# Performance work log

Hardware: AMD Instinct MI355X
Metric: run time of the kernel (lower is better)

Reference implementation:

```python
import jax, jax.numpy as jnp
import numpy as np

MARGIN = 0.3
MIN_POS_DIST = 0.1
PUSH_SCALE = 2.0
DISSIMILAR_REL = 1  # dissimilar_relation_ids == {1}


def setup_inputs() -> dict:
    key = jax.random.key(0)
    k1, k2, k3, k4, k5 = jax.random.split(key, 5)
    B, D = 16384, 1024
    h = jax.random.normal(k1, (B, D), dtype=jnp.float32)
    t = jax.random.normal(k2, (B, D), dtype=jnp.float32)
    r = jax.random.normal(k3, (B, D), dtype=jnp.float32)
    relation_ids = jax.random.randint(k4, (B,), 0, 10, dtype=jnp.int64 if jax.config.jax_enable_x64 else jnp.int32)
    neg = jax.random.randint(k5, (B,), 0, B, dtype=relation_ids.dtype)
    idx = jnp.arange(B, dtype=neg.dtype)
    neg_idx = jnp.where(neg == idx, (neg + 1) % B, neg)  # enforce neg_idx[i] != i
    return {"h": h, "t": t, "r": r, "relation_ids": relation_ids, "neg_idx": neg_idx}


def reference(h, t, r, relation_ids, neg_idx):
    # pos_dist[i] = ||h[i] + r[i] - t[i]||_2
    hr = h + r                                  # [B, D]
    pos_dist = jnp.linalg.norm(hr - t, axis=-1)  # [B]
    # neg_dist[i] = ||h[i] + r[i] - t[neg_idx[i]]||_2
    neg_dist = jnp.linalg.norm(hr - t[neg_idx], axis=-1)  # [B]

    dissim = relation_ids == DISSIMILAR_REL
    curr_margin = MARGIN * PUSH_SCALE
    loss_dissim = jax.nn.relu(curr_margin - pos_dist) + 0.5 * jnp.exp(-pos_dist)
    loss_sim = jax.nn.relu(pos_dist - neg_dist + MARGIN) + 0.3 * jax.nn.relu(MIN_POS_DIST - pos_dist)
    per_sample = jnp.where(dissim, loss_dissim, loss_sim)
    return jnp.mean(per_sample)
```

## Files before the change

### kernel.cpp

```cpp
#include <hip/hip_runtime.h>
#include <math.h>


#define BDIM 16384
#define DDIM 1024

__global__ __launch_bounds__(256) void triplet_rows_kernel(
    const float* __restrict__ h, const float* __restrict__ t,
    const float* __restrict__ r, const int* __restrict__ rel,
    const int* __restrict__ neg, float* __restrict__ per_row)
{
    const int wave = threadIdx.x >> 6;
    const int lane = threadIdx.x & 63;
    const int row  = (blockIdx.x << 2) + wave;

    const float4* h4 = (const float4*)(h + (size_t)row * DDIM);
    const float4* t4 = (const float4*)(t + (size_t)row * DDIM);
    const float4* r4 = (const float4*)(r + (size_t)row * DDIM);
    const int nidx   = neg[row];
    const float4* n4 = (const float4*)(t + (size_t)nidx * DDIM);

    float psum = 0.0f, nsum = 0.0f;
#pragma unroll
    for (int j = 0; j < 4; ++j) {
        const int k = lane + (j << 6);
        float4 hv = h4[k];
        float4 rv = r4[k];
        float4 tv = t4[k];
        float4 nv = n4[k];
        float hrx = hv.x + rv.x, hry = hv.y + rv.y,
              hrz = hv.z + rv.z, hrw = hv.w + rv.w;
        float dx = hrx - tv.x, dy = hry - tv.y,
              dz = hrz - tv.z, dw = hrw - tv.w;
        psum += dx * dx + dy * dy + dz * dz + dw * dw;
        float ex = hrx - nv.x, ey = hry - nv.y,
              ez = hrz - nv.z, ew = hrw - nv.w;
        nsum += ex * ex + ey * ey + ez * ez + ew * ew;
    }

#pragma unroll
    for (int off = 32; off > 0; off >>= 1) {
        psum += __shfl_down(psum, off, 64);
        nsum += __shfl_down(nsum, off, 64);
    }

    if (lane == 0) {
        float pos = sqrtf(psum);
        float negd = sqrtf(nsum);
        float loss;
        if (rel[row] == 1) {
            loss = fmaxf(0.6f - pos, 0.0f) + 0.5f * expf(-pos);
        } else {
            loss = fmaxf(pos - negd + 0.3f, 0.0f)
                 + 0.3f * fmaxf(0.1f - pos, 0.0f);
        }
        per_row[row] = loss;
    }
}

__global__ __launch_bounds__(256) void reduce_mean_kernel(
    const float* __restrict__ per_row, float* __restrict__ out)
{
    __shared__ float sm[4];
    float s = 0.0f;
    for (int i = threadIdx.x; i < BDIM; i += 256)
        s += per_row[i];
#pragma unroll
    for (int off = 32; off > 0; off >>= 1)
        s += __shfl_down(s, off, 64);
    const int lane = threadIdx.x & 63;
    const int wave = threadIdx.x >> 6;
    if (lane == 0) sm[wave] = s;
    __syncthreads();
    if (threadIdx.x == 0)
        out[0] = (sm[0] + sm[1] + sm[2] + sm[3]) * (1.0f / (float)BDIM);
}

extern "C" void kernel_launch(void* const* d_in, const int* in_sizes, int n_in,
                              void* d_out, int out_size, void* d_ws, size_t ws_size,
                              hipStream_t stream) {
    const float* h = (const float*)d_in[0];
    const float* t = (const float*)d_in[1];
    const float* r = (const float*)d_in[2];
    const int* rel = (const int*)d_in[3];
    const int* neg = (const int*)d_in[4];
    float* per_row = (float*)d_ws;
    float* out = (float*)d_out;

    triplet_rows_kernel<<<BDIM / 4, 256, 0, stream>>>(h, t, r, rel, neg, per_row);
    reduce_mean_kernel<<<1, 256, 0, stream>>>(per_row, out);
}
```

Before: 216.4 us.

## Fuse mean reduction via atomics, process two rows per wave, skip unused negative loads

Folds the separate reduce kernel into the row kernel by having each block atomically add its scaled partial sum into the output, which is zeroed by a tiny kernel first. Each wave now handles two rows for more memory-level parallelism per wave. For dissimilar-relation rows, whose loss ignores the negative distance, the negative pointer is aliased to the row's own t, so the random gather of a negative row is replaced by a re-read of data already being fetched. The atomic float accumulation makes the summation order nondeterministic.

Result: faster. 207.3 us (-4.2%).

```diff
diff --git a/kernel.cpp b/kernel.cpp
--- a/kernel.cpp
+++ b/kernel.cpp
@@ -4,76 +4,77 @@
 
 #define BDIM 16384
 #define DDIM 1024
+#define NBLOCK 2048
 
-__global__ __launch_bounds__(256) void triplet_rows_kernel(
+__global__ void zero_out_kernel(float* __restrict__ out) { out[0] = 0.0f; }
+
+__global__ __launch_bounds__(256) void triplet_fused_kernel(
     const float* __restrict__ h, const float* __restrict__ t,
     const float* __restrict__ r, const int* __restrict__ rel,
-    const int* __restrict__ neg, float* __restrict__ per_row)
+    const int* __restrict__ neg, float* __restrict__ out)
 {
     const int wave = threadIdx.x >> 6;
     const int lane = threadIdx.x & 63;
-    const int row  = (blockIdx.x << 2) + wave;
+    const int wid  = (blockIdx.x << 2) + wave;
+    const int row0 = wid << 1;
+    const int row1 = row0 + 1;
 
-    const float4* h4 = (const float4*)(h + (size_t)row * DDIM);
-    const float4* t4 = (const float4*)(t + (size_t)row * DDIM);
-    const float4* r4 = (const float4*)(r + (size_t)row * DDIM);
-    const int nidx   = neg[row];
-    const float4* n4 = (const float4*)(t + (size_t)nidx * DDIM);
+    const float4* h0 = (const float4*)(h + (size_t)row0 * DDIM);
+    const float4* r0 = (const float4*)(r + (size_t)row0 * DDIM);
+    const float4* t0 = (const float4*)(t + (size_t)row0 * DDIM);
+    const float4* h1 = (const float4*)(h + (size_t)row1 * DDIM);
+    const float4* r1 = (const float4*)(r + (size_t)row1 * DDIM);
+    const float4* t1 = (const float4*)(t + (size_t)row1 * DDIM);
 
-    float psum = 0.0f, nsum = 0.0f;
+    const int rel0 = rel[row0];
+    const int rel1 = rel[row1];
+    const float4* n0 = (rel0 == 1) ? t0 : (const float4*)(t + (size_t)neg[row0] * DDIM);
+    const float4* n1 = (rel1 == 1) ? t1 : (const float4*)(t + (size_t)neg[row1] * DDIM);
+
+    float ps0 = 0.0f, ns0 = 0.0f, ps1 = 0.0f, ns1 = 0.0f;
 #pragma unroll
     for (int j = 0; j < 4; ++j) {
         const int k = lane + (j << 6);
-        float4 hv = h4[k];
-        float4 rv = r4[k];
-        float4 tv = t4[k];
-        float4 nv = n4[k];
-        float hrx = hv.x + rv.x, hry = hv.y + rv.y,
-              hrz = hv.z + rv.z, hrw = hv.w + rv.w;
-        float dx = hrx - tv.x, dy = hry - tv.y,
-              dz = hrz - tv.z, dw = hrw - tv.w;
-        psum += dx * dx + dy * dy + dz * dz + dw * dw;
-        float ex = hrx - nv.x, ey = hry - nv.y,
-              ez = hrz - nv.z, ew = hrw - nv.w;
-        nsum += ex * ex + ey * ey + ez * ez + ew * ew;
+        float4 ha = h0[k]; float4 ra = r0[k]; float4 ta = t0[k]; float4 na = n0[k];
+        float4 hb = h1[k]; float4 rb = r1[k]; float4 tb = t1[k]; float4 nb = n1[k];
+
+        float ax = ha.x + ra.x, ay = ha.y + ra.y, az = ha.z + ra.z, aw = ha.w + ra.w;
+        float dx = ax - ta.x, dy = ay - ta.y, dz = az - ta.z, dw = aw - ta.w;
+        ps0 += dx * dx + dy * dy + dz * dz + dw * dw;
+        float ex = ax - na.x, ey = ay - na.y, ez = az - na.z, ew = aw - na.w;
+        ns0 += ex * ex + ey * ey + ez * ez + ew * ew;
+
+        float bx = hb.x + rb.x, by = hb.y + rb.y, bz = hb.z + rb.z, bw = hb.w + rb.w;
+        float fx = bx - tb.x, fy = by - tb.y, fz = bz - tb.z, fw = bw - tb.w;
+        ps1 += fx * fx + fy * fy + fz * fz + fw * fw;
+        float gx = bx - nb.x, gy = by - nb.y, gz = bz - nb.z, gw = bw - nb.w;
+        ns1 += gx * gx + gy * gy + gz * gz + gw * gw;
     }
 
 #pragma unroll
     for (int off = 32; off > 0; off >>= 1) {
-        psum += __shfl_down(psum, off, 64);
-        nsum += __shfl_down(nsum, off, 64);
+        ps0 += __shfl_down(ps0, off, 64);
+        ns0 += __shfl_down(ns0, off, 64);
+        ps1 += __shfl_down(ps1, off, 64);
+        ns1 += __shfl_down(ns1, off, 64);
     }
 
+    __shared__ float sm[4];
     if (lane == 0) {
-        float pos = sqrtf(psum);
-        float negd = sqrtf(nsum);
-        float loss;
-        if (rel[row] == 1) {
-            loss = fmaxf(0.6f - pos, 0.0f) + 0.5f * expf(-pos);
-        } else {
-            loss = fmaxf(pos - negd + 0.3f, 0.0f)
-                 + 0.3f * fmaxf(0.1f - pos, 0.0f);
-        }
-        per_row[row] = loss;
+        float pos0 = sqrtf(ps0), neg0 = sqrtf(ns0);
+        float pos1 = sqrtf(ps1), neg1 = sqrtf(ns1);
+        float l0, l1;
+        if (rel0 == 1) l0 = fmaxf(0.6f - pos0, 0.0f) + 0.5f * expf(-pos0);
+        else           l0 = fmaxf(pos0 - neg0 + 0.3f, 0.0f) + 0.3f * fmaxf(0.1f - pos0, 0.0f);
+        if (rel1 == 1) l1 = fmaxf(0.6f - pos1, 0.0f) + 0.5f * expf(-pos1);
+        else           l1 = fmaxf(pos1 - neg1 + 0.3f, 0.0f) + 0.3f * fmaxf(0.1f - pos1, 0.0f);
+        sm[wave] = l0 + l1;
     }
-}
-
-__global__ __launch_bounds__(256) void reduce_mean_kernel(
-    const float* __restrict__ per_row, float* __restrict__ out)
-{
-    __shared__ float sm[4];
-    float s = 0.0f;
-    for (int i = threadIdx.x; i < BDIM; i += 256)
-        s += per_row[i];
-#pragma unroll
-    for (int off = 32; off > 0; off >>= 1)
-        s += __shfl_down(s, off, 64);
-    const int lane = threadIdx.x & 63;
-    const int wave = threadIdx.x >> 6;
-    if (lane == 0) sm[wave] = s;
     __syncthreads();
-    if (threadIdx.x == 0)
-        out[0] = (sm[0] + sm[1] + sm[2] + sm[3]) * (1.0f / (float)BDIM);
+    if (threadIdx.x == 0) {
+        float blk = (sm[0] + sm[1] + sm[2] + sm[3]) * (1.0f / (float)BDIM);
+        atomicAdd(out, blk);
+    }
 }
 
 extern "C" void kernel_launch(void* const* d_in, const int* in_sizes, int n_in,
@@ -84,9 +85,8 @@
     const float* r = (const float*)d_in[2];
     const int* rel = (const int*)d_in[3];
     const int* neg = (const int*)d_in[4];
-    float* per_row = (float*)d_ws;
     float* out = (float*)d_out;
 
-    triplet_rows_kernel<<<BDIM / 4, 256, 0, stream>>>(h, t, r, rel, neg, per_row);
-    reduce_mean_kernel<<<1, 256, 0, stream>>>(per_row, out);
+    zero_out_kernel<<<1, 1, 0, stream>>>(out);
+    triplet_fused_kernel<<<NBLOCK, 256, 0, stream>>>(h, t, r, rel, neg, out);
 }
```

## Fuse mean reduction into row kernel via atomics and batch all row loads upfront

Applied to the files above, without the earlier changes.

Replaces the separate single-block reduction kernel with a per-block shared-memory sum followed by an atomicAdd into the output, zeroed by a tiny preceding kernel. The row kernel now issues all h, r, t and gathered negative-row loads before any arithmetic, which raises memory-level parallelism, and declares launch bounds with a minimum of two blocks per CU. The aim is to drop the serial reduce kernel and hide load latency better, at the cost of 4096 atomics, nondeterministic summation order and higher register pressure.

Result: faster. 208.0 us (-3.9%).

```diff
diff --git a/kernel.cpp b/kernel.cpp
--- a/kernel.cpp
+++ b/kernel.cpp
@@ -5,36 +5,53 @@
 #define BDIM 16384
 #define DDIM 1024
 
-__global__ __launch_bounds__(256) void triplet_rows_kernel(
+__global__ void zero_out_kernel(float* __restrict__ out) { out[0] = 0.0f; }
+
+__global__ __launch_bounds__(256, 2) void triplet_fused_kernel(
     const float* __restrict__ h, const float* __restrict__ t,
     const float* __restrict__ r, const int* __restrict__ rel,
-    const int* __restrict__ neg, float* __restrict__ per_row)
+    const int* __restrict__ neg, float* __restrict__ out)
 {
     const int wave = threadIdx.x >> 6;
     const int lane = threadIdx.x & 63;
     const int row  = (blockIdx.x << 2) + wave;
 
+    const int nidx = neg[row];
+    const int rl   = rel[row];
+
     const float4* h4 = (const float4*)(h + (size_t)row * DDIM);
+    const float4* r4 = (const float4*)(r + (size_t)row * DDIM);
     const float4* t4 = (const float4*)(t + (size_t)row * DDIM);
-    const float4* r4 = (const float4*)(r + (size_t)row * DDIM);
-    const int nidx   = neg[row];
+
+    float4 H[4], R[4], T[4];
+#pragma unroll
+    for (int j = 0; j < 4; ++j) H[j] = h4[lane + (j << 6)];
+#pragma unroll
+    for (int j = 0; j < 4; ++j) R[j] = r4[lane + (j << 6)];
+#pragma unroll
+    for (int j = 0; j < 4; ++j) T[j] = t4[lane + (j << 6)];
+
     const float4* n4 = (const float4*)(t + (size_t)nidx * DDIM);
+    float4 N[4];
+#pragma unroll
+    for (int j = 0; j < 4; ++j) N[j] = n4[lane + (j << 6)];
 
-    float psum = 0.0f, nsum = 0.0f;
+    float4 HR[4];
+    float psum = 0.0f;
 #pragma unroll
     for (int j = 0; j < 4; ++j) {
-        const int k = lane + (j << 6);
-        float4 hv = h4[k];
-        float4 rv = r4[k];
-        float4 tv = t4[k];
-        float4 nv = n4[k];
-        float hrx = hv.x + rv.x, hry = hv.y + rv.y,
-              hrz = hv.z + rv.z, hrw = hv.w + rv.w;
-        float dx = hrx - tv.x, dy = hry - tv.y,
-              dz = hrz - tv.z, dw = hrw - tv.w;
+        HR[j].x = H[j].x + R[j].x; HR[j].y = H[j].y + R[j].y;
+        HR[j].z = H[j].z + R[j].z; HR[j].w = H[j].w + R[j].w;
+        float dx = HR[j].x - T[j].x, dy = HR[j].y - T[j].y,
+              dz = HR[j].z - T[j].z, dw = HR[j].w - T[j].w;
         psum += dx * dx + dy * dy + dz * dz + dw * dw;
-        float ex = hrx - nv.x, ey = hry - nv.y,
-              ez = hrz - nv.z, ew = hrw - nv.w;
+    }
+
+    float nsum = 0.0f;
+#pragma unroll
+    for (int j = 0; j < 4; ++j) {
+        float ex = HR[j].x - N[j].x, ey = HR[j].y - N[j].y,
+              ez = HR[j].z - N[j].z, ew = HR[j].w - N[j].w;
         nsum += ex * ex + ey * ey + ez * ez + ew * ew;
     }
 
@@ -44,36 +61,21 @@
         nsum += __shfl_down(nsum, off, 64);
     }
 
+    __shared__ float sm[4];
     if (lane == 0) {
         float pos = sqrtf(psum);
         float negd = sqrtf(nsum);
         float loss;
-        if (rel[row] == 1) {
-            loss = fmaxf(0.6f - pos, 0.0f) + 0.5f * expf(-pos);
-        } else {
-            loss = fmaxf(pos - negd + 0.3f, 0.0f)
-                 + 0.3f * fmaxf(0.1f - pos, 0.0f);
-        }
-        per_row[row] = loss;
+        if (rl == 1) loss = fmaxf(0.6f - pos, 0.0f) + 0.5f * expf(-pos);
+        else         loss = fmaxf(pos - negd + 0.3f, 0.0f)
+                          + 0.3f * fmaxf(0.1f - pos, 0.0f);
+        sm[wave] = loss;
     }
-}
-
-__global__ __launch_bounds__(256) void reduce_mean_kernel(
-    const float* __restrict__ per_row, float* __restrict__ out)
-{
-    __shared__ float sm[4];
-    float s = 0.0f;
-    for (int i = threadIdx.x; i < BDIM; i += 256)
-        s += per_row[i];
-#pragma unroll
-    for (int off = 32; off > 0; off >>= 1)
-        s += __shfl_down(s, off, 64);
-    const int lane = threadIdx.x & 63;
-    const int wave = threadIdx.x >> 6;
-    if (lane == 0) sm[wave] = s;
     __syncthreads();
-    if (threadIdx.x == 0)
-        out[0] = (sm[0] + sm[1] + sm[2] + sm[3]) * (1.0f / (float)BDIM);
+    if (threadIdx.x == 0) {
+        float blk = (sm[0] + sm[1] + sm[2] + sm[3]) * (1.0f / (float)BDIM);
+        atomicAdd(out, blk);
+    }
 }
 
 extern "C" void kernel_launch(void* const* d_in, const int* in_sizes, int n_in,
@@ -84,9 +86,8 @@
     const float* r = (const float*)d_in[2];
     const int* rel = (const int*)d_in[3];
     const int* neg = (const int*)d_in[4];
-    float* per_row = (float*)d_ws;
     float* out = (float*)d_out;
 
-    triplet_rows_kernel<<<BDIM / 4, 256, 0, stream>>>(h, t, r, rel, neg, per_row);
-    reduce_mean_kernel<<<1, 256, 0, stream>>>(per_row, out);
+    zero_out_kernel<<<1, 1, 0, stream>>>(out);
+    triplet_fused_kernel<<<BDIM / 4, 256, 0, stream>>>(h, t, r, rel, neg, out);
 }
```
